# Performance work log

Hardware: AMD Instinct MI355X
Metric: run time of the kernel (lower is better)

The kernel has to match this reference:

```python
import jax, jax.numpy as jnp
import numpy as np

C0 = 32          # cs[0] == cs[1] with planes=[32,32,...], cr=1.0
CIN = 4
EPS = 1e-5

# ---------- host-side coordinate hashing (mirrors F.sphash / F.sphashquery) ----------

def _enc(c):
    # unique int64 code per (x,y,z); +2 shift keeps offset-adjusted coords positive
    return (c[:, 0] + 2).astype(np.int64) + (c[:, 1] + 2).astype(np.int64) * 1024 \
        + (c[:, 2] + 2).astype(np.int64) * 1024 * 1024

def _lookup(sorted_codes, q):
    pos = np.searchsorted(sorted_codes, q)
    pos = np.minimum(pos, len(sorted_codes) - 1)
    return np.where(sorted_codes[pos] == q, pos, -1).astype(np.int32)

def _offsets(r):
    return np.array([[i, j, k] for i in r for j in r for k in r], np.int64)


def setup_inputs() -> dict:
    rng = np.random.default_rng(0)
    N0 = 400000
    pts = rng.integers(0, [400, 400, 40], size=(600000, 3)).astype(np.int64)
    codes = _enc(pts)
    codes_u, idx = np.unique(codes, return_index=True)
    assert len(codes_u) >= N0
    coords0, codes0 = pts[idx][:N0], codes_u[:N0]   # sorted by hash code

    off27, off8 = _offsets([-1, 0, 1]), _offsets([0, 1])
    # ks=3 stride=1 kernel map at level 0: nbr0[k, i] = index of coords0[i]+off27[k] (or -1)
    nbr0 = np.stack([_lookup(codes0, _enc(coords0 + o)) for o in off27])

    # stride-2 downsample coords (level 1)
    c1all = coords0 // 2
    codes1_u, i1 = np.unique(_enc(c1all), return_index=True)
    coords1 = c1all[i1]
    # ks=2 stride=2 kernel map: output voxel gathers inputs at 2*out + {0,1}^3
    down1 = np.stack([_lookup(codes0, _enc(coords1 * 2 + o)) for o in off8])
    # ks=3 stride=1 kernel map at level 1
    nbr1 = np.stack([_lookup(codes1_u, _enc(coords1 + o)) for o in off27])

    key = jax.random.key(0)
    ks = jax.random.split(key, 10)

    def w(k, K, ci, co):
        return jax.random.normal(k, (K, ci, co), jnp.float32) * (1.0 / np.sqrt(K * ci))

    return {
        "voxel_features": jax.random.normal(ks[0], (N0, CIN), jnp.float32),
        "W_stem1": w(ks[1], 27, CIN, C0),
        "W_stem2": w(ks[2], 27, C0, C0),
        "W_down":  w(ks[3], 8,  C0, C0),
        "W_r1a":   w(ks[4], 27, C0, C0),
        "W_r1b":   w(ks[5], 27, C0, C0),
        "W_r2a":   w(ks[6], 27, C0, C0),
        "W_r2b":   w(ks[7], 27, C0, C0),
        "gammas": jnp.ones((7, C0), jnp.float32),
        "betas":  jnp.zeros((7, C0), jnp.float32),
        "nbr0":  jnp.asarray(nbr0),
        "down1": jnp.asarray(down1),
        "nbr1":  jnp.asarray(nbr1),
    }


# ---------- sparse conv: gather-GEMM-scatter per kernel offset ----------

def _spconv(feat, nbr, W):
    # feat [N, Ci], nbr [K, M] (-1 = no neighbor), W [K, Ci, Co] -> out [M, Co]
    def step(acc, kw):
        idx, Wk = kw
        g = jnp.where((idx >= 0)[:, None], feat[jnp.maximum(idx, 0)], 0.0)
        return acc + g @ Wk, None
    acc0 = jnp.zeros((nbr.shape[1], W.shape[-1]), feat.dtype)
    out, _ = jax.lax.scan(step, acc0, (nbr, W))
    return out


def _bn(x, g, b):
    # BatchNorm1d, training-mode statistics (biased var), gamma/beta affine
    mu = x.mean(0)
    var = x.var(0)
    return (x - mu) * jax.lax.rsqrt(var + EPS) * g + b


def _cbr(x, nbr, W, g, b):
    return jax.nn.relu(_bn(_spconv(x, nbr, W), g, b))


def reference(voxel_features, W_stem1, W_stem2, W_down, W_r1a, W_r1b, W_r2a, W_r2b,
              gammas, betas, nbr0, down1, nbr1):
    g, b = gammas, betas
    # stem: two ks=3 sparse convs + BN + ReLU at level 0
    x = _cbr(voxel_features, nbr0, W_stem1, g[0], b[0])
    x = _cbr(x, nbr0, W_stem2, g[1], b[1])
    # stage1: BasicConvolutionBlock (ks=2, stride=2) + 2 ResidualBlocks at level 1
    x1 = _cbr(x, down1, W_down, g[2], b[2])
    h = _cbr(x1, nbr1, W_r1a, g[3], b[3])
    h = _bn(_spconv(h, nbr1, W_r1b), g[4], b[4])
    x1 = jax.nn.relu(h + x1)          # downsample == Identity (inc == outc, stride 1)
    h = _cbr(x1, nbr1, W_r2a, g[5], b[5])
    h = _bn(_spconv(h, nbr1, W_r2b), g[6], b[6])
    return jax.nn.relu(h + x1)
```

## Files before the change

kernel.cpp:

```cpp
#include <hip/hip_runtime.h>

#define EPS 1e-5f
#define WROWS 448

typedef __attribute__((ext_vector_type(8))) short short8;
typedef __attribute__((ext_vector_type(4))) float floatx4;
typedef __attribute__((ext_vector_type(8))) unsigned short ushort8;
typedef __attribute__((ext_vector_type(4))) unsigned short ushortv4;

#define O_S1  0
#define O_S2  4096
#define O_DN  (O_S2 + 27648)
#define O_R1A (O_DN + 8192)
#define O_R1B (O_R1A + 27648)
#define O_R2A (O_R1B + 27648)
#define O_R2B (O_R2A + 27648)
#define WP_TOTAL (O_R2B + 27648)

__device__ __forceinline__ unsigned short f2bf(float f) {
    union { float f; unsigned u; } x; x.f = f;
    unsigned r = x.u + 0x7fffu + ((x.u >> 16) & 1u);
    return (unsigned short)(r >> 16);
}
__device__ __forceinline__ float bf2f(unsigned short b) {
    union { unsigned u; float f; } x; x.u = ((unsigned)b) << 16;
    return x.f;
}

__device__ __forceinline__ int xcd_swizzle(int nb) {
    int b = (int)blockIdx.x;
    int q = nb >> 3, r = nb & 7;
    int x = b & 7, i = b >> 3;
    return x * q + (x < r ? x : r) + i;
}

__device__ __forceinline__ short8 gath(const unsigned short* __restrict__ x,
                                       int ii, int q) {
    short8 z = {};
    return (ii >= 0) ? *(const short8*)(x + (size_t)ii * 32 + q * 8) : z;
}

__device__ __forceinline__ void pack_w_one(
    const float* __restrict__ W, unsigned short* __restrict__ out, int t)
{
    int lane = t & 63;
    int h = (t >> 6) & 1;
    int k = t >> 7;
    int m = lane & 15, q = lane >> 4;
    ushort8 v;
#pragma unroll
    for (int j = 0; j < 8; ++j)
        v[j] = f2bf(W[((size_t)k * 32 + q * 8 + j) * 32 + h * 16 + m]);
    *(ushort8*)(out + (size_t)t * 8) = v;
}

__global__ __launch_bounds__(256) void prep_kernel(
    const float* __restrict__ vf,
    const float* __restrict__ Ws1, const float* __restrict__ Ws2,
    const float* __restrict__ Wd,  const float* __restrict__ Wr1a,
    const float* __restrict__ Wr1b, const float* __restrict__ Wr2a,
    const float* __restrict__ Wr2b,
    unsigned short* __restrict__ xb, unsigned short* __restrict__ wp, int N0)
{
    int t = blockIdx.x * 256 + threadIdx.x;
    if (t < N0) {
        float4 v = *(const float4*)(vf + (size_t)t * 4);
        ushortv4 r = {f2bf(v.x), f2bf(v.y), f2bf(v.z), f2bf(v.w)};
        *(ushortv4*)(xb + (size_t)t * 4) = r;
        return;
    }
    t -= N0;
    if (t < 512) {
        int lane = t & 63;
        int h = (t >> 6) & 1;
        int c = t >> 7;
        int m = lane & 15, q = lane >> 4;
        ushort8 v;
#pragma unroll
        for (int j = 0; j < 8; ++j) {
            int kdim = c * 32 + q * 8 + j;
            int tap = kdim >> 2, ci = kdim & 3;
            v[j] = (tap < 27) ? f2bf(Ws1[((size_t)tap * 4 + ci) * 32 + h * 16 + m]) : 0;
        }
        *(ushort8*)(wp + O_S1 + (size_t)t * 8) = v;
        return;
    }
    t -= 512;
    if (t < 27 * 128) { pack_w_one(Ws2,  wp + O_S2,  t); return; }
    t -= 27 * 128;
    if (t < 8 * 128)  { pack_w_one(Wd,   wp + O_DN,  t); return; }
    t -= 8 * 128;
    if (t < 27 * 128) { pack_w_one(Wr1a, wp + O_R1A, t); return; }
    t -= 27 * 128;
    if (t < 27 * 128) { pack_w_one(Wr1b, wp + O_R1B, t); return; }
    t -= 27 * 128;
    if (t < 27 * 128) { pack_w_one(Wr2a, wp + O_R2A, t); return; }
    t -= 27 * 128;
    if (t < 27 * 128) { pack_w_one(Wr2b, wp + O_R2B, t); return; }
}

__device__ __forceinline__ void conv_epilogue2(
    floatx4 acc00, floatx4 acc01, floatx4 acc10, floatx4 acc11,
    unsigned short* __restrict__ y, float* __restrict__ part,
    int rowbase, int lb, int N, float* sm)
{
    const int lane = threadIdx.x & 63;
    const int m = lane & 15, q = lane >> 4;

    if (threadIdx.x < 64) sm[threadIdx.x] = 0.f;
    __syncthreads();

#pragma unroll
    for (int r = 0; r < 4; ++r) {
        int ra = rowbase + q * 4 + r;
        int rb = ra + 16;
        if (ra < N) {
            y[(size_t)ra * 32 + m]      = f2bf(acc00[r]);
            y[(size_t)ra * 32 + 16 + m] = f2bf(acc01[r]);
        }
        if (rb < N) {
            y[(size_t)rb * 32 + m]      = f2bf(acc10[r]);
            y[(size_t)rb * 32 + 16 + m] = f2bf(acc11[r]);
        }
    }

    float s0 = 0.f, q0 = 0.f, s1 = 0.f, q1 = 0.f;
#pragma unroll
    for (int r = 0; r < 4; ++r) {
        s0 += acc00[r] + acc10[r];
        q0 += acc00[r] * acc00[r] + acc10[r] * acc10[r];
        s1 += acc01[r] + acc11[r];
        q1 += acc01[r] * acc01[r] + acc11[r] * acc11[r];
    }
    s0 += __shfl_down(s0, 32); s0 += __shfl_down(s0, 16);
    q0 += __shfl_down(q0, 32); q0 += __shfl_down(q0, 16);
    s1 += __shfl_down(s1, 32); s1 += __shfl_down(s1, 16);
    q1 += __shfl_down(q1, 32); q1 += __shfl_down(q1, 16);
    if (lane < 16) {
        atomicAdd(&sm[m],      s0);
        atomicAdd(&sm[32 + m], q0);
        atomicAdd(&sm[16 + m],      s1);
        atomicAdd(&sm[48 + m], q1);
    }
    __syncthreads();
    if (threadIdx.x < 64)
        part[(size_t)lb * 64 + threadIdx.x] = sm[threadIdx.x];
}

#define MFMA_BF16 __builtin_amdgcn_mfma_f32_16x16x32_bf16

template <int K>
__global__ __launch_bounds__(256) void conv_mfma_kernel(
    const unsigned short* __restrict__ x,
    const int* __restrict__ nbr,
    const unsigned short* __restrict__ Wp,
    unsigned short* __restrict__ y,
    float* __restrict__ part, int N)
{
    constexpr int ZG  = (K == 27) ? 3 : 2;
    constexpr int TPG = (K == 27) ? 9 : 4;

    __shared__ __align__(16) unsigned short win[WROWS * 40];
    __shared__ float sm[64];
    __shared__ int wmm[2 * 3];

    const int nb = (N + 127) / 128;
    const int lb = xcd_swizzle(nb);
    const int lane = threadIdx.x & 63;
    const int wave = threadIdx.x >> 6;
    const int m = lane & 15, q = lane >> 4;
    const int rowbase = lb * 128 + wave * 32;
    const int r0 = rowbase + m;
    const int r1 = r0 + 16;
    const bool v0 = r0 < N, v1 = r1 < N;

    floatx4 c00 = {0.f, 0.f, 0.f, 0.f};
    floatx4 c01 = c00, c10 = c00, c11 = c00;

    if (threadIdx.x < 2 * ZG)
        wmm[threadIdx.x] = (threadIdx.x & 1) ? -1 : 0x7fffffff;
    __syncthreads();

#define IDX(k, rr, vv) ((vv) ? nbr[(size_t)(k) * N + (rr)] : -1)
#define LG(ii) ({ short8 z_ = {}; \
    (ii) >= 0 ? *(const short8*)(&win[((ii) - wmin) * 40 + q * 8]) : z_; })
#define MN(a) ((a) < 0 ? 0x7fffffff : (a))

    for (int c = 0; c < ZG; ++c) {
        int ia0 = (0 < TPG) ? IDX(c + ZG * 0, r0, v0) : -1;
        int ib0 = (0 < TPG) ? IDX(c + ZG * 0, r1, v1) : -1;
        int ia1 = (1 < TPG) ? IDX(c + ZG * 1, r0, v0) : -1;
        int ib1 = (1 < TPG) ? IDX(c + ZG * 1, r1, v1) : -1;
        int ia2 = (2 < TPG) ? IDX(c + ZG * 2, r0, v0) : -1;
        int ib2 = (2 < TPG) ? IDX(c + ZG * 2, r1, v1) : -1;
        int ia3 = (3 < TPG) ? IDX(c + ZG * 3, r0, v0) : -1;
        int ib3 = (3 < TPG) ? IDX(c + ZG * 3, r1, v1) : -1;
        int ia4 = (4 < TPG) ? IDX(c + ZG * 4, r0, v0) : -1;
        int ib4 = (4 < TPG) ? IDX(c + ZG * 4, r1, v1) : -1;
        int ia5 = (5 < TPG) ? IDX(c + ZG * 5, r0, v0) : -1;
        int ib5 = (5 < TPG) ? IDX(c + ZG * 5, r1, v1) : -1;
        int ia6 = (6 < TPG) ? IDX(c + ZG * 6, r0, v0) : -1;
        int ib6 = (6 < TPG) ? IDX(c + ZG * 6, r1, v1) : -1;
        int ia7 = (7 < TPG) ? IDX(c + ZG * 7, r0, v0) : -1;
        int ib7 = (7 < TPG) ? IDX(c + ZG * 7, r1, v1) : -1;
        int ia8 = (8 < TPG) ? IDX(c + ZG * 8, r0, v0) : -1;
        int ib8 = (8 < TPG) ? IDX(c + ZG * 8, r1, v1) : -1;

        int lmin = min(min(min(min(MN(ia0), MN(ib0)), min(MN(ia1), MN(ib1))),
                           min(min(MN(ia2), MN(ib2)), min(MN(ia3), MN(ib3)))),
                       min(min(min(MN(ia4), MN(ib4)), min(MN(ia5), MN(ib5))),
                           min(min(MN(ia6), MN(ib6)),
                               min(min(MN(ia7), MN(ib7)), min(MN(ia8), MN(ib8))))));
        int lmax = max(max(max(max(ia0, ib0), max(ia1, ib1)),
                           max(max(ia2, ib2), max(ia3, ib3))),
                       max(max(max(ia4, ib4), max(ia5, ib5)),
                           max(max(ia6, ib6), max(max(ia7, ib7), max(ia8, ib8)))));
#pragma unroll
        for (int off = 32; off >= 1; off >>= 1) {
            lmin = min(lmin, __shfl_down(lmin, off));
            lmax = max(lmax, __shfl_down(lmax, off));
        }
        if (lane == 0) { atomicMin(&wmm[2 * c], lmin); atomicMax(&wmm[2 * c + 1], lmax); }
        __syncthreads();

        const int wmin = wmm[2 * c];
        const int wmax = wmm[2 * c + 1];
        const bool any = (wmax >= 0);
        const int wspan = wmax - wmin + 1;
        const bool use_lds = any && (wspan <= WROWS);

        if (use_lds) {
            const short8* src = (const short8*)(x + (size_t)wmin * 32);
            for (int cc = threadIdx.x; cc < wspan * 4; cc += 256) {
                int rr = cc >> 2, hh = cc & 3;
                *(short8*)&win[rr * 40 + hh * 8] = src[cc];
            }
        }
        __syncthreads();

#define TAPC(J, iA, iB)                                                   \
        if (J < TPG) {                                                    \
            const short8* wk = (const short8*)(Wp + (size_t)(c + ZG * J) * 1024); \
            short8 b0 = wk[lane];                                         \
            short8 b1 = wk[64 + lane];                                    \
            short8 a0, a1;                                                \
            if (use_lds) { a0 = LG(iA); a1 = LG(iB); }                    \
            else         { a0 = gath(x, iA, q); a1 = gath(x, iB, q); }    \
            c00 = MFMA_BF16(a0, b0, c00, 0, 0, 0);                        \
            c01 = MFMA_BF16(a0, b1, c01, 0, 0, 0);                        \
            c10 = MFMA_BF16(a1, b0, c10, 0, 0, 0);                        \
            c11 = MFMA_BF16(a1, b1, c11, 0, 0, 0);                        \
        }
        if (any) {
            TAPC(0, ia0, ib0) TAPC(1, ia1, ib1) TAPC(2, ia2, ib2)
            TAPC(3, ia3, ib3) TAPC(4, ia4, ib4) TAPC(5, ia5, ib5)
            TAPC(6, ia6, ib6) TAPC(7, ia7, ib7) TAPC(8, ia8, ib8)
        }
#undef TAPC
    }
#undef IDX
#undef LG
#undef MN

    conv_epilogue2(c00, c01, c10, c11, y, part, rowbase, lb, N, sm);
}

__global__ __launch_bounds__(256) void conv_stem1_mfma(
    const unsigned short* __restrict__ xb,
    const int* __restrict__ nbr,
    const unsigned short* __restrict__ Wp,
    unsigned short* __restrict__ y,
    float* __restrict__ part, int N)
{
    __shared__ float sm[64];
    const int nb = (N + 127) / 128;
    const int lb = xcd_swizzle(nb);
    const int lane = threadIdx.x & 63;
    const int wave = threadIdx.x >> 6;
    const int m = lane & 15, q = lane >> 4;
    const int rowbase = lb * 128 + wave * 32;
    const int row0 = rowbase + m;
    const int row1 = rowbase + 16 + m;

    floatx4 acc00 = {0.f, 0.f, 0.f, 0.f};
    floatx4 acc01 = acc00, acc10 = acc00, acc11 = acc00;

#pragma unroll
    for (int c = 0; c < 4; ++c) {
        const int t0 = c * 8 + q * 2, t1 = t0 + 1;
        short8 a0 = {}, a1 = {};
        {
            int ia = (t0 < 27 && row0 < N) ? nbr[(size_t)t0 * N + row0] : -1;
            int ib = (t1 < 27 && row0 < N) ? nbr[(size_t)t1 * N + row0] : -1;
            ushortv4 ga = {}, gb = {};
            if (ia >= 0) ga = *(const ushortv4*)(xb + (size_t)ia * 4);
            if (ib >= 0) gb = *(const ushortv4*)(xb + (size_t)ib * 4);
            a0[0] = (short)ga[0]; a0[1] = (short)ga[1];
            a0[2] = (short)ga[2]; a0[3] = (short)ga[3];
            a0[4] = (short)gb[0]; a0[5] = (short)gb[1];
            a0[6] = (short)gb[2]; a0[7] = (short)gb[3];
        }
        {
            int ia = (t0 < 27 && row1 < N) ? nbr[(size_t)t0 * N + row1] : -1;
            int ib = (t1 < 27 && row1 < N) ? nbr[(size_t)t1 * N + row1] : -1;
            ushortv4 ga = {}, gb = {};
            if (ia >= 0) ga = *(const ushortv4*)(xb + (size_t)ia * 4);
            if (ib >= 0) gb = *(const ushortv4*)(xb + (size_t)ib * 4);
            a1[0] = (short)ga[0]; a1[1] = (short)ga[1];
            a1[2] = (short)ga[2]; a1[3] = (short)ga[3];
            a1[4] = (short)gb[0]; a1[5] = (short)gb[1];
            a1[6] = (short)gb[2]; a1[7] = (short)gb[3];
        }
        const short8* wk = (const short8*)Wp;
        short8 b0 = wk[(c * 2 + 0) * 64 + lane];
        short8 b1 = wk[(c * 2 + 1) * 64 + lane];
        acc00 = MFMA_BF16(a0, b0, acc00, 0, 0, 0);
        acc01 = MFMA_BF16(a0, b1, acc01, 0, 0, 0);
        acc10 = MFMA_BF16(a1, b0, acc10, 0, 0, 0);
        acc11 = MFMA_BF16(a1, b1, acc11, 0, 0, 0);
    }

    conv_epilogue2(acc00, acc01, acc10, acc11, y, part, rowbase, lb, N, sm);
}

__global__ __launch_bounds__(256) void reduce_stats_kernel(
    const float* __restrict__ part, float* __restrict__ stats, int nb)
{
    __shared__ float sm[256];
    int t = threadIdx.x;
    int c = t & 63, g = t >> 6;
    float s = 0.f;
    for (int b = blockIdx.x * 4 + g; b < nb; b += 256)
        s += part[(size_t)b * 64 + c];
    sm[t] = s;
    __syncthreads();
    if (t < 64)
        atomicAdd(&stats[t], sm[t] + sm[64 + t] + sm[128 + t] + sm[192 + t]);
}

template <bool OUT_F32, bool HAS_RES>
__global__ __launch_bounds__(256) void bn_relu_kernel(
    const unsigned short* __restrict__ y, const float* __restrict__ stats,
    const float* __restrict__ gamma, const float* __restrict__ beta,
    const unsigned short* __restrict__ resid, void* __restrict__ outp, int N)
{
    int t = blockIdx.x * 256 + threadIdx.x;
    if (t >= N) return;
    float inv_n = 1.0f / (float)N;
    const ushort8* yr = (const ushort8*)(y + (size_t)t * 32);

#pragma unroll
    for (int c = 0; c < 4; ++c) {
        ushort8 v = yr[c];
        ushort8 rv = {};
        if (HAS_RES) rv = ((const ushort8*)(resid + (size_t)t * 32))[c];
        float f0, f1, f2, f3, f4, f5, f6, f7;
#define BNJ(fj, j)                                                        \
        {                                                                 \
            int co = c * 8 + (j);                                         \
            float mu = stats[co] * inv_n;                                 \
            float var = stats[32 + co] * inv_n - mu * mu;                 \
            float sc = rsqrtf(var + EPS) * gamma[co];                     \
            fj = (bf2f(v[j]) - mu) * sc + beta[co];                       \
            if (HAS_RES) fj += bf2f(rv[j]);                               \
            fj = fmaxf(fj, 0.0f);                                         \
        }
        BNJ(f0, 0) BNJ(f1, 1) BNJ(f2, 2) BNJ(f3, 3)
        BNJ(f4, 4) BNJ(f5, 5) BNJ(f6, 6) BNJ(f7, 7)
#undef BNJ
        if (OUT_F32) {
            float* ob = (float*)outp + (size_t)t * 32 + c * 8;
            floatx4 u0 = {f0, f1, f2, f3}, u1 = {f4, f5, f6, f7};
            *(floatx4*)(ob) = u0;
            *(floatx4*)(ob + 4) = u1;
        } else {
            ushort8 o;
            o[0] = f2bf(f0); o[1] = f2bf(f1); o[2] = f2bf(f2); o[3] = f2bf(f3);
            o[4] = f2bf(f4); o[5] = f2bf(f5); o[6] = f2bf(f6); o[7] = f2bf(f7);
            ((ushort8*)((unsigned short*)outp + (size_t)t * 32))[c] = o;
        }
    }
}

extern "C" void kernel_launch(void* const* d_in, const int* in_sizes, int n_in,
                              void* d_out, int out_size, void* d_ws, size_t ws_size,
                              hipStream_t stream)
{
    const float* vf   = (const float*)d_in[0];
    const float* Ws1  = (const float*)d_in[1];
    const float* Ws2  = (const float*)d_in[2];
    const float* Wd   = (const float*)d_in[3];
    const float* Wr1a = (const float*)d_in[4];
    const float* Wr1b = (const float*)d_in[5];
    const float* Wr2a = (const float*)d_in[6];
    const float* Wr2b = (const float*)d_in[7];
    const float* gam  = (const float*)d_in[8];
    const float* bet  = (const float*)d_in[9];
    const int* nbr0   = (const int*)d_in[10];
    const int* down1  = (const int*)d_in[11];
    const int* nbr1   = (const int*)d_in[12];

    int N0 = in_sizes[0] / 4;
    int N1 = in_sizes[11] / 8;

    unsigned short* yraw = (unsigned short*)d_ws;
    unsigned short* actA = yraw + (size_t)N0 * 32;
    unsigned short* actB = actA + (size_t)N0 * 32;
    unsigned short* xb   = actB + (size_t)N0 * 32;
    unsigned short* wp   = xb + (size_t)N0 * 4;
    float* part  = (float*)(wp + WP_TOTAL);
    float* stats = part + (size_t)3200 * 64;

    hipMemsetAsync(stats, 0, 7 * 64 * sizeof(float), stream);

    auto g1 = [](int n) { return dim3((unsigned)((n + 255) / 256)); };
    auto gm = [](int n) { return dim3((unsigned)((n + 127) / 128)); };
    int nb0 = (N0 + 127) / 128;
    int nb1 = (N1 + 127) / 128;

    int prep_threads = N0 + 512 + 128 * (27 * 5 + 8);
    prep_kernel<<<g1(prep_threads), 256, 0, stream>>>(
        vf, Ws1, Ws2, Wd, Wr1a, Wr1b, Wr2a, Wr2b, xb, wp, N0);

    conv_stem1_mfma<<<gm(N0), 256, 0, stream>>>(xb, nbr0, wp + O_S1, yraw, part, N0);
    reduce_stats_kernel<<<64, 256, 0, stream>>>(part, stats + 0 * 64, nb0);
    bn_relu_kernel<false, false><<<g1(N0), 256, 0, stream>>>(yraw, stats + 0 * 64, gam + 0, bet + 0, nullptr, actA, N0);
    conv_mfma_kernel<27><<<gm(N0), 256, 0, stream>>>(actA, nbr0, wp + O_S2, yraw, part, N0);
    reduce_stats_kernel<<<64, 256, 0, stream>>>(part, stats + 1 * 64, nb0);
    bn_relu_kernel<false, false><<<g1(N0), 256, 0, stream>>>(yraw, stats + 1 * 64, gam + 32, bet + 32, nullptr, actB, N0);
    conv_mfma_kernel<8><<<gm(N1), 256, 0, stream>>>(actB, down1, wp + O_DN, yraw, part, N1);
    reduce_stats_kernel<<<64, 256, 0, stream>>>(part, stats + 2 * 64, nb1);
    bn_relu_kernel<false, false><<<g1(N1), 256, 0, stream>>>(yraw, stats + 2 * 64, gam + 64, bet + 64, nullptr, actA, N1);
    conv_mfma_kernel<27><<<gm(N1), 256, 0, stream>>>(actA, nbr1, wp + O_R1A, yraw, part, N1);
    reduce_stats_kernel<<<64, 256, 0, stream>>>(part, stats + 3 * 64, nb1);
    bn_relu_kernel<false, false><<<g1(N1), 256, 0, stream>>>(yraw, stats + 3 * 64, gam + 96, bet + 96, nullptr, actB, N1);
    conv_mfma_kernel<27><<<gm(N1), 256, 0, stream>>>(actB, nbr1, wp + O_R1B, yraw, part, N1);
    reduce_stats_kernel<<<64, 256, 0, stream>>>(part, stats + 4 * 64, nb1);
    bn_relu_kernel<false, true><<<g1(N1), 256, 0, stream>>>(yraw, stats + 4 * 64, gam + 128, bet + 128, actA, actB, N1);
    conv_mfma_kernel<27><<<gm(N1), 256, 0, stream>>>(actB, nbr1, wp + O_R2A, yraw, part, N1);
    reduce_stats_kernel<<<64, 256, 0, stream>>>(part, stats + 5 * 64, nb1);
    bn_relu_kernel<false, false><<<g1(N1), 256, 0, stream>>>(yraw, stats + 5 * 64, gam + 160, bet + 160, nullptr, actA, N1);
    conv_mfma_kernel<27><<<gm(N1), 256, 0, stream>>>(actA, nbr1, wp + O_R2B, yraw, part, N1);
    reduce_stats_kernel<<<64, 256, 0, stream>>>(part, stats + 6 * 64, nb1);
    bn_relu_kernel<true, true><<<g1(N1), 256, 0, stream>>>(yraw, stats + 6 * 64, gam + 192, bet + 192, actB, d_out, N1);
}
```

Measured before the change: 635.3 us.

## Precompute gather windows in prep and stage them into LDS with async global_load_lds

Result: slower. 699.4 us (+10.1%).

```diff
diff --git a/kernel.cpp b/kernel.cpp
--- a/kernel.cpp
+++ b/kernel.cpp
@@ -17,6 +17,11 @@
 #define O_R2B (O_R2A + 27648)
 #define WP_TOTAL (O_R2B + 27648)
 
+#define GLL16(g, l)                                                       \
+    __builtin_amdgcn_global_load_lds(                                     \
+        (const __attribute__((address_space(1))) void*)(g),               \
+        (__attribute__((address_space(3))) void*)(l), 16, 0, 0)
+
 __device__ __forceinline__ unsigned short f2bf(float f) {
     union { float f; unsigned u; } x; x.f = f;
     unsigned r = x.u + 0x7fffu + ((x.u >> 16) & 1u);
@@ -38,6 +43,33 @@
                                        int ii, int q) {
     short8 z = {};
     return (ii >= 0) ? *(const short8*)(x + (size_t)ii * 32 + q * 8) : z;
+}
+
+template <int ZG, int TPG>
+__device__ __forceinline__ void wmm_calc(
+    const int* __restrict__ nbr, int N, int t, int* __restrict__ out)
+{
+    int ln = t & 63, wv = t >> 6;
+    int lb = wv / ZG, c = wv - lb * ZG;
+    int base = lb * 128;
+    int mn = 0x7fffffff, mx = -1;
+#pragma unroll
+    for (int j = 0; j < TPG; ++j) {
+#pragma unroll
+        for (int h = 0; h < 2; ++h) {
+            int r = base + h * 64 + ln;
+            if (r < N) {
+                int v = nbr[(size_t)(c + ZG * j) * N + r];
+                if (v >= 0) { mn = min(mn, v); mx = max(mx, v); }
+            }
+        }
+    }
+#pragma unroll
+    for (int off = 32; off >= 1; off >>= 1) {
+        mn = min(mn, __shfl_down(mn, off));
+        mx = max(mx, __shfl_down(mx, off));
+    }
+    if (ln == 0) { out[wv * 2] = (mx < 0) ? 0 : mn; out[wv * 2 + 1] = mx; }
 }
 
 __device__ __forceinline__ void pack_w_one(
@@ -60,7 +92,11 @@
     const float* __restrict__ Wd,  const float* __restrict__ Wr1a,
     const float* __restrict__ Wr1b, const float* __restrict__ Wr2a,
     const float* __restrict__ Wr2b,
-    unsigned short* __restrict__ xb, unsigned short* __restrict__ wp, int N0)
+    const int* __restrict__ nbr0, const int* __restrict__ down1,
+    const int* __restrict__ nbr1,
+    unsigned short* __restrict__ xb, unsigned short* __restrict__ wp,
+    int* __restrict__ wmm0, int* __restrict__ wmmD, int* __restrict__ wmm1,
+    int N0, int N1)
 {
     int t = blockIdx.x * 256 + threadIdx.x;
     if (t < N0) {
@@ -97,6 +133,13 @@
     if (t < 27 * 128) { pack_w_one(Wr2a, wp + O_R2A, t); return; }
     t -= 27 * 128;
     if (t < 27 * 128) { pack_w_one(Wr2b, wp + O_R2B, t); return; }
+    t -= 27 * 128;
+    int nb0 = (N0 + 127) >> 7, nb1 = (N1 + 127) >> 7;
+    if (t < nb0 * 3 * 64) { wmm_calc<3, 9>(nbr0, N0, t, wmm0); return; }
+    t -= nb0 * 3 * 64;
+    if (t < nb1 * 2 * 64) { wmm_calc<2, 4>(down1, N1, t, wmmD); return; }
+    t -= nb1 * 2 * 64;
+    if (t < nb1 * 3 * 64) { wmm_calc<3, 9>(nbr1, N1, t, wmm1); return; }
 }
 
 __device__ __forceinline__ void conv_epilogue2(
@@ -150,21 +193,21 @@
 #define MFMA_BF16 __builtin_amdgcn_mfma_f32_16x16x32_bf16
 
 template <int K>
-__global__ __launch_bounds__(256) void conv_mfma_kernel(
+__global__ __launch_bounds__(256, 5) void conv_mfma_kernel(
     const unsigned short* __restrict__ x,
     const int* __restrict__ nbr,
     const unsigned short* __restrict__ Wp,
+    const int* __restrict__ wmmg,
     unsigned short* __restrict__ y,
     float* __restrict__ part, int N)
 {
     constexpr int ZG  = (K == 27) ? 3 : 2;
     constexpr int TPG = (K == 27) ? 9 : 4;
 
-    __shared__ __align__(16) unsigned short win[WROWS * 40];
+    __shared__ __align__(16) unsigned short win[WROWS * 32];
     __shared__ float sm[64];
-    __shared__ int wmm[2 * 3];
-
-    const int nb = (N + 127) / 128;
+
+    const int nb = (N + 127) >> 7;
     const int lb = xcd_swizzle(nb);
     const int lane = threadIdx.x & 63;
     const int wave = threadIdx.x >> 6;
@@ -177,16 +220,41 @@
     floatx4 c00 = {0.f, 0.f, 0.f, 0.f};
     floatx4 c01 = c00, c10 = c00, c11 = c00;
 
-    if (threadIdx.x < 2 * ZG)
-        wmm[threadIdx.x] = (threadIdx.x & 1) ? -1 : 0x7fffffff;
-    __syncthreads();
+    int wmn[ZG], wc4[ZG];
+#pragma unroll
+    for (int c = 0; c < ZG; ++c) {
+        int lo = wmmg[(lb * ZG + c) * 2];
+        int hi = wmmg[(lb * ZG + c) * 2 + 1];
+        wmn[c] = lo;
+        int sp = (hi < 0) ? 0 : (hi - lo + 1);
+        wc4[c] = (sp < WROWS ? sp : WROWS) * 4;
+    }
 
 #define IDX(k, rr, vv) ((vv) ? nbr[(size_t)(k) * N + (rr)] : -1)
-#define LG(ii) ({ short8 z_ = {}; \
-    (ii) >= 0 ? *(const short8*)(&win[((ii) - wmin) * 40 + q * 8]) : z_; })
-#define MN(a) ((a) < 0 ? 0x7fffffff : (a))
+#define LOADA(dst, ii)                                                     \
+    {                                                                      \
+        unsigned rr_ = (unsigned)((ii) - wmin);                            \
+        unsigned rc_ = rr_ < (unsigned)WROWS ? rr_ : (unsigned)(WROWS - 1);\
+        dst = *(const short8*)&win[rc_ * 32 + ((q ^ ((rc_ >> 1) & 3)) << 3)]; \
+        if (__any((ii) >= 0 && rr_ >= (unsigned)WROWS)) {                  \
+            if ((ii) >= 0 && rr_ >= (unsigned)WROWS)                       \
+                dst = *(const short8*)(x + (size_t)(ii) * 32 + q * 8);     \
+        }                                                                  \
+        if ((ii) < 0) { short8 z_ = {}; dst = z_; }                        \
+    }
 
     for (int c = 0; c < ZG; ++c) {
+        const int wmin = wmn[c];
+        const int sc4 = wc4[c];
+
+        for (int cb = wave * 64; cb < sc4; cb += 256) {
+            int cc = cb + lane;
+            int rr = cc >> 2, s = cc & 3;
+            int qq = s ^ ((rr >> 1) & 3);
+            if (cc < sc4)
+                GLL16(x + ((size_t)(wmin + rr)) * 32 + qq * 8, win + (size_t)cb * 8);
+        }
+
         int ia0 = (0 < TPG) ? IDX(c + ZG * 0, r0, v0) : -1;
         int ib0 = (0 < TPG) ? IDX(c + ZG * 0, r1, v1) : -1;
         int ia1 = (1 < TPG) ? IDX(c + ZG * 1, r0, v0) : -1;
@@ -206,61 +274,36 @@
         int ia8 = (8 < TPG) ? IDX(c + ZG * 8, r0, v0) : -1;
         int ib8 = (8 < TPG) ? IDX(c + ZG * 8, r1, v1) : -1;
 
-        int lmin = min(min(min(min(MN(ia0), MN(ib0)), min(MN(ia1), MN(ib1))),
-                           min(min(MN(ia2), MN(ib2)), min(MN(ia3), MN(ib3)))),
-                       min(min(min(MN(ia4), MN(ib4)), min(MN(ia5), MN(ib5))),
-                           min(min(MN(ia6), MN(ib6)),
-                               min(min(MN(ia7), MN(ib7)), min(MN(ia8), MN(ib8))))));
-        int lmax = max(max(max(max(ia0, ib0), max(ia1, ib1)),
-                           max(max(ia2, ib2), max(ia3, ib3))),
-                       max(max(max(ia4, ib4), max(ia5, ib5)),
-                           max(max(ia6, ib6), max(max(ia7, ib7), max(ia8, ib8)))));
-#pragma unroll
-        for (int off = 32; off >= 1; off >>= 1) {
-            lmin = min(lmin, __shfl_down(lmin, off));
-            lmax = max(lmax, __shfl_down(lmax, off));
-        }
-        if (lane == 0) { atomicMin(&wmm[2 * c], lmin); atomicMax(&wmm[2 * c + 1], lmax); }
         __syncthreads();
 
-        const int wmin = wmm[2 * c];
-        const int wmax = wmm[2 * c + 1];
-        const bool any = (wmax >= 0);
-        const int wspan = wmax - wmin + 1;
-        const bool use_lds = any && (wspan <= WROWS);
-
-        if (use_lds) {
-            const short8* src = (const short8*)(x + (size_t)wmin * 32);
-            for (int cc = threadIdx.x; cc < wspan * 4; cc += 256) {
-                int rr = cc >> 2, hh = cc & 3;
-                *(short8*)&win[rr * 40 + hh * 8] = src[cc];
-            }
-        }
-        __syncthreads();
-
-#define TAPC(J, iA, iB)                                                   \
-        if (J < TPG) {                                                    \
-            const short8* wk = (const short8*)(Wp + (size_t)(c + ZG * J) * 1024); \
-            short8 b0 = wk[lane];                                         \
-            short8 b1 = wk[64 + lane];                                    \
-            short8 a0, a1;                                                \
-            if (use_lds) { a0 = LG(iA); a1 = LG(iB); }                    \
-            else         { a0 = gath(x, iA, q); a1 = gath(x, iB, q); }    \
-            c00 = MFMA_BF16(a0, b0, c00, 0, 0, 0);                        \
-            c01 = MFMA_BF16(a0, b1, c01, 0, 0, 0);                        \
-            c10 = MFMA_BF16(a1, b0, c10, 0, 0, 0);                        \
-            c11 = MFMA_BF16(a1, b1, c11, 0, 0, 0);                        \
-        }
-        if (any) {
-            TAPC(0, ia0, ib0) TAPC(1, ia1, ib1) TAPC(2, ia2, ib2)
-            TAPC(3, ia3, ib3) TAPC(4, ia4, ib4) TAPC(5, ia5, ib5)
-            TAPC(6, ia6, ib6) TAPC(7, ia7, ib7) TAPC(8, ia8, ib8)
-        }
+#define TAPC(J, iA, iB)                                                    \
+        if (J < TPG) {                                                     \
+            bool sA = __all((iA) < 0), sB = __all((iB) < 0);               \
+            if (!(sA && sB)) {                                             \
+                const short8* wk = (const short8*)(Wp + (size_t)(c + ZG * J) * 1024); \
+                short8 b0 = wk[lane];                                      \
+                short8 b1 = wk[64 + lane];                                 \
+                if (!sA) {                                                 \
+                    short8 a0; LOADA(a0, iA);                              \
+                    c00 = MFMA_BF16(a0, b0, c00, 0, 0, 0);                 \
+                    c01 = MFMA_BF16(a0, b1, c01, 0, 0, 0);                 \
+                }                                                          \
+                if (!sB) {                                                 \
+                    short8 a1; LOADA(a1, iB);                              \
+                    c10 = MFMA_BF16(a1, b0, c10, 0, 0, 0);                 \
+                    c11 = MFMA_BF16(a1, b1, c11, 0, 0, 0);                 \
+                }                                                          \
+            }                                                              \
+        }
+        TAPC(0, ia0, ib0) TAPC(1, ia1, ib1) TAPC(2, ia2, ib2)
+        TAPC(3, ia3, ib3) TAPC(4, ia4, ib4) TAPC(5, ia5, ib5)
+        TAPC(6, ia6, ib6) TAPC(7, ia7, ib7) TAPC(8, ia8, ib8)
 #undef TAPC
+
+        if (c != ZG - 1) __syncthreads();
     }
 #undef IDX
-#undef LG
-#undef MN
+#undef LOADA
 
     conv_epilogue2(c00, c01, c10, c11, y, part, rowbase, lb, N, sm);
 }
@@ -410,37 +453,41 @@
     unsigned short* wp   = xb + (size_t)N0 * 4;
     float* part  = (float*)(wp + WP_TOTAL);
     float* stats = part + (size_t)3200 * 64;
+    int nb0 = (N0 + 127) / 128;
+    int nb1 = (N1 + 127) / 128;
+    int* wmm0 = (int*)(stats + 7 * 64);
+    int* wmmD = wmm0 + (size_t)nb0 * 6;
+    int* wmm1 = wmmD + (size_t)nb1 * 4;
 
     hipMemsetAsync(stats, 0, 7 * 64 * sizeof(float), stream);
 
     auto g1 = [](int n) { return dim3((unsigned)((n + 255) / 256)); };
     auto gm = [](int n) { return dim3((unsigned)((n + 127) / 128)); };
-    int nb0 = (N0 + 127) / 128;
-    int nb1 = (N1 + 127) / 128;
-
-    int prep_threads = N0 + 512 + 128 * (27 * 5 + 8);
+
+    int prep_threads = N0 + 512 + 128 * (27 * 5 + 8) + 64 * (nb0 * 3 + nb1 * 5);
     prep_kernel<<<g1(prep_threads), 256, 0, stream>>>(
-        vf, Ws1, Ws2, Wd, Wr1a, Wr1b, Wr2a, Wr2b, xb, wp, N0);
+        vf, Ws1, Ws2, Wd, Wr1a, Wr1b, Wr2a, Wr2b,
+        nbr0, down1, nbr1, xb, wp, wmm0, wmmD, wmm1, N0, N1);
 
     conv_stem1_mfma<<<gm(N0), 256, 0, stream>>>(xb, nbr0, wp + O_S1, yraw, part, N0);
     reduce_stats_kernel<<<64, 256, 0, stream>>>(part, stats + 0 * 64, nb0);
     bn_relu_kernel<false, false><<<g1(N0), 256, 0, stream>>>(yraw, stats + 0 * 64, gam + 0, bet + 0, nullptr, actA, N0);
-    conv_mfma_kernel<27><<<gm(N0), 256, 0, stream>>>(actA, nbr0, wp + O_S2, yraw, part, N0);
+    conv_mfma_kernel<27><<<gm(N0), 256, 0, stream>>>(actA, nbr0, wp + O_S2, wmm0, yraw, part, N0);
     reduce_stats_kernel<<<64, 256, 0, stream>>>(part, stats + 1 * 64, nb0);
     bn_relu_kernel<false, false><<<g1(N0), 256, 0, stream>>>(yraw, stats + 1 * 64, gam + 32, bet + 32, nullptr, actB, N0);
-    conv_mfma_kernel<8><<<gm(N1), 256, 0, stream>>>(actB, down1, wp + O_DN, yraw, part, N1);
+    conv_mfma_kernel<8><<<gm(N1), 256, 0, stream>>>(actB, down1, wp + O_DN, wmmD, yraw, part, N1);
     reduce_stats_kernel<<<64, 256, 0, stream>>>(part, stats + 2 * 64, nb1);
     bn_relu_kernel<false, false><<<g1(N1), 256, 0, stream>>>(yraw, stats + 2 * 64, gam + 64, bet + 64, nullptr, actA, N1);
-    conv_mfma_kernel<27><<<gm(N1), 256, 0, stream>>>(actA, nbr1, wp + O_R1A, yraw, part, N1);
+    conv_mfma_kernel<27><<<gm(N1), 256, 0, stream>>>(actA, nbr1, wp + O_R1A, wmm1, yraw, part, N1);
     reduce_stats_kernel<<<64, 256, 0, stream>>>(part, stats + 3 * 64, nb1);
     bn_relu_kernel<false, false><<<g1(N1), 256, 0, stream>>>(yraw, stats + 3 * 64, gam + 96, bet + 96, nullptr, actB, N1);
-    conv_mfma_kernel<27><<<gm(N1), 256, 0, stream>>>(actB, nbr1, wp + O_R1B, yraw, part, N1);
+    conv_mfma_kernel<27><<<gm(N1), 256, 0, stream>>>(actB, nbr1, wp + O_R1B, wmm1, yraw, part, N1);
     reduce_stats_kernel<<<64, 256, 0, stream>>>(part, stats + 4 * 64, nb1);
     bn_relu_kernel<false, true><<<g1(N1), 256, 0, stream>>>(yraw, stats + 4 * 64, gam + 128, bet + 128, actA, actB, N1);
-    conv_mfma_kernel<27><<<gm(N1), 256, 0, stream>>>(actB, nbr1, wp + O_R2A, yraw, part, N1);
+    conv_mfma_kernel<27><<<gm(N1), 256, 0, stream>>>(actB, nbr1, wp + O_R2A, wmm1, yraw, part, N1);
     reduce_stats_kernel<<<64, 256, 0, stream>>>(part, stats + 5 * 64, nb1);
     bn_relu_kernel<false, false><<<g1(N1), 256, 0, stream>>>(yraw, stats + 5 * 64, gam + 160, bet + 160, nullptr, actA, N1);
-    conv_mfma_kernel<27><<<gm(N1), 256, 0, stream>>>(actA, nbr1, wp + O_R2B, yraw, part, N1);
+    conv_mfma_kernel<27><<<gm(N1), 256, 0, stream>>>(actA, nbr1, wp + O_R2B, wmm1, yraw, part, N1);
     reduce_stats_kernel<<<64, 256, 0, stream>>>(part, stats + 6 * 64, nb1);
     bn_relu_kernel<true, true><<<g1(N1), 256, 0, stream>>>(yraw, stats + 6 * 64, gam + 192, bet + 192, actB, d_out, N1);
 }
```
